# Optimization experiments

Measured on AMD Instinct MI355X. Metric: run time of the kernel, lower is better.

The kernel has to match this reference:

```python
import jax, jax.numpy as jnp
import numpy as np

N = 100_000   # nodes
E = 1_600_000 # edges
V = 100_000   # vocab
G = 256       # graphs in batch
D = 64        # emb/hidden dim


def setup_inputs() -> dict:
    key = jax.random.key(0)
    ks = jax.random.split(key, 12)
    x_tokens = jax.random.randint(ks[0], (N, 1), 0, V)
    edge_index = jax.random.randint(ks[1], (2, E), 0, N)
    batch = jnp.sort(jax.random.randint(ks[2], (N,), 0, G))
    s = 0.02
    return {
        "x_tokens": x_tokens,
        "edge_index": edge_index,
        "batch": batch,
        "emb_table": jax.random.normal(ks[3], (V, D), jnp.float32) * s,
        "W0": jax.random.normal(ks[4], (D, D), jnp.float32) * s,
        "b0": jnp.zeros((D,), jnp.float32),
        "W1": jax.random.normal(ks[5], (D, D), jnp.float32) * s,
        "b1": jnp.zeros((D,), jnp.float32),
        "W2": jax.random.normal(ks[6], (D, D), jnp.float32) * s,
        "b2": jnp.zeros((D,), jnp.float32),
        "Wc1": jax.random.normal(ks[7], (2 * D, D), jnp.float32) * s,
        "bc1": jnp.zeros((D,), jnp.float32),
        "Wc2": jax.random.normal(ks[8], (D, 2), jnp.float32) * s,
        "bc2": jnp.zeros((2,), jnp.float32),
    }


def _gcn_norm(edge_index, n_nodes):
    # add self loops, compute symmetric normalization coefficients
    loop = jnp.arange(n_nodes, dtype=edge_index.dtype)
    src = jnp.concatenate([edge_index[0], loop])
    dst = jnp.concatenate([edge_index[1], loop])
    deg = jax.ops.segment_sum(jnp.ones_like(dst, jnp.float32), dst, num_segments=n_nodes)
    dinv = jnp.where(deg > 0, deg ** -0.5, 0.0)
    norm = dinv[src] * dinv[dst]  # [E+N]
    return src, dst, norm


def _gcn_conv(x, W, b, src, dst, norm, n_nodes):
    x = x @ W                                   # [N, D]
    msg = x[src] * norm[:, None]                # gather + scale, [E+N, D]
    out = jax.ops.segment_sum(msg, dst, num_segments=n_nodes)
    return out + b


def reference(x_tokens, edge_index, batch, emb_table, W0, b0, W1, b1, W2, b2, Wc1, bc1, Wc2, bc2):
    n = x_tokens.shape[0]
    src, dst, norm = _gcn_norm(edge_index, n)
    x = emb_table[x_tokens[:, 0]]               # [N, D]
    for W, b in ((W0, b0), (W1, b1), (W2, b2)):
        x = jax.nn.relu(_gcn_conv(x, W, b, src, dst, norm, n))
    # dual pooling over graph ids
    cnt = jax.ops.segment_sum(jnp.ones((n,), x.dtype), batch, num_segments=G)
    h_sum = jax.ops.segment_sum(x, batch, num_segments=G)
    h_mean = h_sum / jnp.maximum(cnt, 1.0)[:, None]
    h_max = jax.ops.segment_max(x, batch, num_segments=G)
    h_max = jnp.where(jnp.isfinite(h_max), h_max, 0.0)
    h = jnp.concatenate([h_mean, h_max], axis=-1)   # [G, 2D]
    logits = jax.nn.relu(h @ Wc1 + bc1) @ Wc2 + bc2  # [G, 2]
    return logits
```

## Files before the change

### kernel.cpp

```cpp
#include <hip/hip_runtime.h>
#include <hip/hip_fp16.h>
#include <math.h>


#define BKT_LOG 9
#define BKT (1 << BKT_LOG)
#define CHUNK 4096

typedef _Float16 h2 __attribute__((ext_vector_type(2)));
typedef _Float16 f16x4 __attribute__((ext_vector_type(4)));
typedef _Float16 f16x8 __attribute__((ext_vector_type(8)));
typedef float f32x4 __attribute__((ext_vector_type(4)));

union HU { unsigned u; h2 h; };
__device__ inline h2 h2bits(unsigned u) { HU x; x.u = u; return x.h; }

#if __has_builtin(__builtin_amdgcn_fdot2)
#define FDOT2(a, b, c) __builtin_amdgcn_fdot2((a), (b), (c), false)
#else
__device__ inline float FDOT2(h2 a, h2 b, float c) {
  return (float)a.x * (float)b.x + (float)a.y * (float)b.y + c;
}
#endif

#define MASK_X 0x00003C00u
#define MASK_Y 0x3C000000u

__device__ inline void acc4c(uint2 v, float& a0, float& a1, float& a2, float& a3) {
  h2 lo = h2bits(v.x), hi = h2bits(v.y);
  a0 = FDOT2(lo, h2bits(MASK_X), a0);
  a1 = FDOT2(lo, h2bits(MASK_Y), a1);
  a2 = FDOT2(hi, h2bits(MASK_X), a2);
  a3 = FDOT2(hi, h2bits(MASK_Y), a3);
}

__global__ __launch_bounds__(256) void k_wcvt(const float* __restrict__ W0,
                                              const float* __restrict__ W1,
                                              const float* __restrict__ W2,
                                              _Float16* __restrict__ Wf,
                                              int* __restrict__ gcur,
                                              float* __restrict__ hz, int hzn) {
  if (blockIdx.x < 3) {
    const float* W = (blockIdx.x == 0) ? W0 : (blockIdx.x == 1) ? W1 : W2;
    _Float16* out = Wf + blockIdx.x * 4096;
    for (int i = threadIdx.x; i < 4096; i += 256) {
      int c = i >> 10, s = (i >> 9) & 1, l = (i >> 3) & 63, j = i & 7;
      int k = 32 * s + 8 * (l >> 4) + j;
      int ncol = 16 * c + (l & 15);
      out[i] = (_Float16)W[k * 64 + ncol];
    }
  } else if (blockIdx.x == 3) {
    gcur[threadIdx.x] = 0;
  } else {
    for (int i = threadIdx.x; i < hzn; i += 256) hz[i] = 0.f;
  }
}

__global__ __launch_bounds__(256) void k_part(const int* __restrict__ src,
                                              const int* __restrict__ dst,
                                              int* __restrict__ gcur,
                                              int* __restrict__ ebuf,
                                              int E, int S) {
  __shared__ int sA[CHUNK];
  __shared__ int dA[CHUNK];
  __shared__ int h[256], base[256];
  int tid = threadIdx.x;
  long c0 = (long)blockIdx.x * CHUNK;
  int m = (int)min((long)CHUNK, (long)E - c0);
  h[tid] = 0;
  __syncthreads();
  for (int i = tid; i < m; i += 256) {
    int s = src[c0 + i];
    int d = dst[c0 + i];
    sA[i] = s;
    dA[i] = d;
    atomicAdd(&h[d >> BKT_LOG], 1);
  }
  __syncthreads();
  if (h[tid]) base[tid] = atomicAdd(&gcur[tid], h[tid]);
  __syncthreads();
  h[tid] = 0;
  __syncthreads();
  for (int i = tid; i < m; i += 256) {
    int s = sA[i], d = dA[i];
    int k = d >> BKT_LOG;
    int p = base[k] + atomicAdd(&h[k], 1);
    if (p < S)
      ebuf[k * S + p] = ((d & (BKT - 1)) << 17) | s;
  }
}

__global__ __launch_bounds__(512) void k_bplace(const int* __restrict__ ebuf,
                                                const int* __restrict__ gcur,
                                                int* __restrict__ off,
                                                int* __restrict__ eend,
                                                int* __restrict__ csrc,
                                                float* __restrict__ dinv,
                                                int N, int S) {
  __shared__ int s[512];
  __shared__ int cur[512];
  int b = blockIdx.x, tid = threadIdx.x;
  int n0 = b << BKT_LOG;
  int nn = min(BKT, N - n0);
  int e0 = b * S;
  int cnt = min(gcur[b], S - nn);
  s[tid] = (tid < nn) ? 1 : 0;
  __syncthreads();
  for (int e = tid; e < cnt; e += 512) atomicAdd(&s[ebuf[e0 + e] >> 17], 1);
  __syncthreads();
  int degws = s[tid];
  for (int d = 1; d < 512; d <<= 1) {
    int t = (tid >= d) ? s[tid - d] : 0;
    __syncthreads();
    s[tid] += t;
    __syncthreads();
  }
  int excl = s[tid] - degws;
  if (tid < nn) {
    off[n0 + tid] = e0 + excl;
    eend[n0 + tid] = e0 + excl + degws;
    dinv[n0 + tid] = 1.0f / sqrtf((float)degws);
    csrc[e0 + excl] = n0 + tid;
  }
  cur[tid] = excl + ((tid < nn) ? 1 : 0);
  __syncthreads();
  for (int e = tid; e < cnt; e += 512) {
    int p = ebuf[e0 + e];
    int pos = e0 + atomicAdd(&cur[p >> 17], 1);
    csrc[pos] = p & 0x1FFFF;
  }
}

template <bool EMB>
__global__ __launch_bounds__(256) void k_mfmamm(const _Float16* __restrict__ y,
                                                const int* __restrict__ tok,
                                                const float* __restrict__ emb,
                                                const _Float16* __restrict__ Wf,
                                                const float* __restrict__ dinv,
                                                float scale,
                                                _Float16* __restrict__ xh,
                                                int n) {
  __shared__ _Float16 lds[4 * 16 * 72];
  int w = threadIdx.x >> 6, l = threadIdx.x & 63;
  int m = l & 15, q = l >> 4;
  int rbase = blockIdx.x * 64 + w * 16;

  f16x8 a0, a1;
  if (EMB) {
    int node = min(rbase + m, n - 1);
    const float* er = emb + (size_t)tok[node] * 64;
    float4 v0 = *(const float4*)(er + q * 8);
    float4 v1 = *(const float4*)(er + q * 8 + 4);
    float4 v2 = *(const float4*)(er + 32 + q * 8);
    float4 v3 = *(const float4*)(er + 32 + q * 8 + 4);
    a0[0] = (_Float16)v0.x; a0[1] = (_Float16)v0.y; a0[2] = (_Float16)v0.z; a0[3] = (_Float16)v0.w;
    a0[4] = (_Float16)v1.x; a0[5] = (_Float16)v1.y; a0[6] = (_Float16)v1.z; a0[7] = (_Float16)v1.w;
    a1[0] = (_Float16)v2.x; a1[1] = (_Float16)v2.y; a1[2] = (_Float16)v2.z; a1[3] = (_Float16)v2.w;
    a1[4] = (_Float16)v3.x; a1[5] = (_Float16)v3.y; a1[6] = (_Float16)v3.z; a1[7] = (_Float16)v3.w;
  } else {
    int node = rbase + m;
    const _Float16* yr = y + ((size_t)(unsigned)node << 6);
    a0 = *(const f16x8*)(yr + q * 8);
    a1 = *(const f16x8*)(yr + 32 + q * 8);
  }
  float4 d4 = *(const float4*)(dinv + rbase + q * 4);

  const f16x8* wf = (const f16x8*)Wf + l;
  f32x4 acc[4];
#pragma unroll
  for (int c = 0; c < 4; c++) {
    f32x4 z = {0.f, 0.f, 0.f, 0.f};
    z = __builtin_amdgcn_mfma_f32_16x16x32_f16(a0, wf[(c * 2 + 0) * 64], z, 0, 0, 0);
    z = __builtin_amdgcn_mfma_f32_16x16x32_f16(a1, wf[(c * 2 + 1) * 64], z, 0, 0, 0);
    acc[c] = z;
  }

  const float ds[4] = {d4.x * scale, d4.y * scale, d4.z * scale, d4.w * scale};
  _Float16* ldw = lds + w * 16 * 72;
#pragma unroll
  for (int c = 0; c < 4; c++)
#pragma unroll
    for (int r = 0; r < 4; r++)
      ldw[(q * 4 + r) * 72 + c * 16 + m] = (_Float16)(acc[c][r] * ds[r]);
  __syncthreads();

  int row2 = l & 15, c2 = l >> 4;
  int node = rbase + row2;
  if (node < n) {
    const uint4* s4 = (const uint4*)(ldw + row2 * 72 + c2 * 16);
    uint4 v0 = s4[0], v1 = s4[1];
    uint4* dst = (uint4*)(xh + ((size_t)(unsigned)node << 6) + c2 * 16);
    dst[0] = v0;
    dst[1] = v1;
  }
}

__global__ __launch_bounds__(256) void k_aggregate(const int* __restrict__ off,
                                                   const int* __restrict__ eend,
                                                   const int* __restrict__ csrc,
                                                   const float* __restrict__ dinv,
                                                   const _Float16* __restrict__ xh,
                                                   const float* __restrict__ bias,
                                                   _Float16* __restrict__ outp,
                                                   int n) {
  int lane = threadIdx.x & 63;
  int t = blockIdx.x * 4 + (threadIdx.x >> 6);
  if (t >= n) return;
  int e0 = off[t];
  int e1 = eend[t];
  int p = lane >> 4;
  int f = lane & 15;
  const char* xb = (const char*)xh;

  float a0 = 0.f, a1 = 0.f, a2 = 0.f, a3 = 0.f;
  for (int base = (e0 & ~7); base < e1; base += 32) {
    int my = base + p * 8;
    int4 iA = {0, 0, 0, 0}, iB = {0, 0, 0, 0};
    if (my < e1) iA = *(const int4*)(csrc + my);
    if (my + 4 < e1) iB = *(const int4*)(csrc + my + 4);
    uint2 v0 = {0,0}, v1 = {0,0}, v2 = {0,0}, v3 = {0,0};
    uint2 v4 = {0,0}, v5 = {0,0}, v6 = {0,0}, v7 = {0,0};
    if (my + 0 >= e0 && my + 0 < e1) v0 = *(const uint2*)(xb + ((size_t)(unsigned)iA.x << 7) + f * 8);
    if (my + 1 >= e0 && my + 1 < e1) v1 = *(const uint2*)(xb + ((size_t)(unsigned)iA.y << 7) + f * 8);
    if (my + 2 >= e0 && my + 2 < e1) v2 = *(const uint2*)(xb + ((size_t)(unsigned)iA.z << 7) + f * 8);
    if (my + 3 >= e0 && my + 3 < e1) v3 = *(const uint2*)(xb + ((size_t)(unsigned)iA.w << 7) + f * 8);
    if (my + 4 >= e0 && my + 4 < e1) v4 = *(const uint2*)(xb + ((size_t)(unsigned)iB.x << 7) + f * 8);
    if (my + 5 >= e0 && my + 5 < e1) v5 = *(const uint2*)(xb + ((size_t)(unsigned)iB.y << 7) + f * 8);
    if (my + 6 >= e0 && my + 6 < e1) v6 = *(const uint2*)(xb + ((size_t)(unsigned)iB.z << 7) + f * 8);
    if (my + 7 >= e0 && my + 7 < e1) v7 = *(const uint2*)(xb + ((size_t)(unsigned)iB.w << 7) + f * 8);
    acc4c(v0, a0, a1, a2, a3);
    acc4c(v1, a0, a1, a2, a3);
    acc4c(v2, a0, a1, a2, a3);
    acc4c(v3, a0, a1, a2, a3);
    acc4c(v4, a0, a1, a2, a3);
    acc4c(v5, a0, a1, a2, a3);
    acc4c(v6, a0, a1, a2, a3);
    acc4c(v7, a0, a1, a2, a3);
  }

  a0 += __shfl_xor(a0, 16); a0 += __shfl_xor(a0, 32);
  a1 += __shfl_xor(a1, 16); a1 += __shfl_xor(a1, 32);
  a2 += __shfl_xor(a2, 16); a2 += __shfl_xor(a2, 32);
  a3 += __shfl_xor(a3, 16); a3 += __shfl_xor(a3, 32);

  if (p == 0) {
    float sc = dinv[t] * (1.0f / 256.0f);
    float4 bb = *(const float4*)(bias + f * 4);
    f16x4 hv;
    hv[0] = (_Float16)(fmaxf(a0 * sc + bb.x, 0.f) * 4096.f);
    hv[1] = (_Float16)(fmaxf(a1 * sc + bb.y, 0.f) * 4096.f);
    hv[2] = (_Float16)(fmaxf(a2 * sc + bb.z, 0.f) * 4096.f);
    hv[3] = (_Float16)(fmaxf(a3 * sc + bb.w, 0.f) * 4096.f);
    *(f16x4*)((char*)outp + ((size_t)(unsigned)t << 7) + f * 8) = hv;
  }
}

__global__ __launch_bounds__(256) void k_pool(const _Float16* __restrict__ x,
                                              const int* __restrict__ batch,
                                              float* __restrict__ hsum,
                                              float* __restrict__ hmax,
                                              int* __restrict__ cntg,
                                              int n) {
  int wid = (blockIdx.x * blockDim.x + threadIdx.x) >> 6;
  int lane = threadIdx.x & 63;
  int i0 = wid * 64;
  if (i0 >= n) return;
  int i1 = min(i0 + 64, n);
  int batch_l = (i0 + lane < n) ? batch[i0 + lane] : 0;
  float gsum = 0.f, gmax = 0.f;
  int cur = __shfl(batch_l, 0);
  int c = 0;
  for (int i = i0; i < i1; i++) {
    int g = __shfl(batch_l, i - i0);
    if (g != cur) {
      atomicAdd(&hsum[cur * 64 + lane], gsum);
      atomicMax((int*)&hmax[cur * 64 + lane], __float_as_int(gmax));
      if (lane == 0) atomicAdd(&cntg[cur], c);
      gsum = 0.f; gmax = 0.f; c = 0; cur = g;
    }
    float v = (float)x[((size_t)(unsigned)i << 6) + lane];
    gsum += v;
    gmax = fmaxf(gmax, v);
    c++;
  }
  atomicAdd(&hsum[cur * 64 + lane], gsum);
  atomicMax((int*)&hmax[cur * 64 + lane], __float_as_int(gmax));
  if (lane == 0) atomicAdd(&cntg[cur], c);
}

__global__ __launch_bounds__(64) void k_cls(const float* __restrict__ hsum,
                                            const float* __restrict__ hmax,
                                            const int* __restrict__ cnt,
                                            const float* __restrict__ Wc1,
                                            const float* __restrict__ bc1,
                                            const float* __restrict__ Wc2,
                                            const float* __restrict__ bc2,
                                            float* __restrict__ out) {
  __shared__ float h[128];
  __shared__ float hid[64];
  int g = blockIdx.x, j = threadIdx.x;
  int c = cnt[g];
  float cf = (float)(c > 0 ? c : 1);
  h[j] = hsum[g * 64 + j] / cf * (1.0f / 4096.0f);
  h[64 + j] = hmax[g * 64 + j] * (1.0f / 4096.0f);
  __syncthreads();
  float acc = bc1[j];
  for (int k = 0; k < 128; k++) acc += h[k] * Wc1[k * 64 + j];
  hid[j] = fmaxf(acc, 0.f);
  __syncthreads();
  if (j < 2) {
    float a = bc2[j];
    for (int k = 0; k < 64; k++) a += hid[k] * Wc2[k * 2 + j];
    out[g * 2 + j] = a;
  }
}

extern "C" void kernel_launch(void* const* d_in, const int* in_sizes, int n_in,
                              void* d_out, int out_size, void* d_ws, size_t ws_size,
                              hipStream_t stream) {
  const int N = in_sizes[0];
  const int E = in_sizes[1] / 2;
  const int G = out_size / 2;
  const int B = (N + BKT - 1) >> BKT_LOG;
  const int Npad = (N + 63) & ~63;
  const int S = ((((E + B - 1) / B) * 3 / 2 + 256) + 7) & ~7;

  const int* tok   = (const int*)d_in[0];
  const int* ei    = (const int*)d_in[1];
  const int* batch = (const int*)d_in[2];
  const float* emb = (const float*)d_in[3];
  const float* W0 = (const float*)d_in[4];  const float* b0 = (const float*)d_in[5];
  const float* W1 = (const float*)d_in[6];  const float* b1 = (const float*)d_in[7];
  const float* W2 = (const float*)d_in[8];  const float* b2 = (const float*)d_in[9];
  const float* Wc1 = (const float*)d_in[10]; const float* bc1 = (const float*)d_in[11];
  const float* Wc2 = (const float*)d_in[12]; const float* bc2 = (const float*)d_in[13];
  const int* srcp = ei;
  const int* dstp = ei + E;

  int* off    = (int*)d_ws;
  int* eend   = off + N;
  float* dinv = (float*)(eend + N);
  int* gcur   = (int*)(dinv + Npad);
  _Float16* Wf = (_Float16*)(gcur + 256);
  int* csrc   = (int*)(Wf + 3 * 4096);
  _Float16* xh = (_Float16*)(csrc + (size_t)B * S);
  _Float16* y  = xh + (size_t)Npad * 64;
  int* ebuf   = (int*)y;
  float* hsum = (float*)(y + (size_t)Npad * 64);
  float* hmax = hsum + (size_t)G * 64;
  int*   cntg = (int*)(hmax + (size_t)G * 64);

  auto cdiv = [](long a, long b) { return (int)((a + b - 1) / b); };
  const int aggBlocks = cdiv(N, 4);

  k_wcvt<<<5, 256, 0, stream>>>(W0, W1, W2, Wf, gcur, hsum, G * 129);

  k_part<<<cdiv(E, CHUNK), 256, 0, stream>>>(srcp, dstp, gcur, ebuf, E, S);
  k_bplace<<<B, 512, 0, stream>>>(ebuf, gcur, off, eend, csrc, dinv, N, S);

  k_mfmamm<true><<<cdiv(N, 64), 256, 0, stream>>>(nullptr, tok, emb, Wf, dinv, 256.f, xh, N);
  k_aggregate<<<aggBlocks, 256, 0, stream>>>(off, eend, csrc, dinv, xh, b0, y, N);

  k_mfmamm<false><<<cdiv(N, 64), 256, 0, stream>>>(y, nullptr, nullptr, Wf + 4096, dinv, 1.f / 16.f, xh, N);
  k_aggregate<<<aggBlocks, 256, 0, stream>>>(off, eend, csrc, dinv, xh, b1, y, N);

  k_mfmamm<false><<<cdiv(N, 64), 256, 0, stream>>>(y, nullptr, nullptr, Wf + 8192, dinv, 1.f / 16.f, xh, N);
  k_aggregate<<<aggBlocks, 256, 0, stream>>>(off, eend, csrc, dinv, xh, b2, y, N);

  k_pool<<<cdiv(N, 256), 256, 0, stream>>>(y, batch, hsum, hmax, cntg, N);

  k_cls<<<G, 64, 0, stream>>>(hsum, hmax, cntg, Wc1, bc1, Wc2, bc2, (float*)d_out);
}
```

Baseline: 332.3 us.

## Locally sort edges by bucket in k_part and split aggregate launches in halves

After: 345.1 us. +3.8%, slower.

```diff
diff --git a/kernel.cpp b/kernel.cpp
--- a/kernel.cpp
+++ b/kernel.cpp
@@ -61,9 +61,10 @@
                                               int* __restrict__ gcur,
                                               int* __restrict__ ebuf,
                                               int E, int S) {
-  __shared__ int sA[CHUNK];
-  __shared__ int dA[CHUNK];
-  __shared__ int h[256], base[256];
+  __shared__ int pk[CHUNK];
+  __shared__ unsigned short bk[CHUNK];
+  __shared__ unsigned short sp[CHUNK];
+  __shared__ int h[256], sc[256], base[256], cur[256];
   int tid = threadIdx.x;
   long c0 = (long)blockIdx.x * CHUNK;
   int m = (int)min((long)CHUNK, (long)E - c0);
@@ -72,21 +73,37 @@
   for (int i = tid; i < m; i += 256) {
     int s = src[c0 + i];
     int d = dst[c0 + i];
-    sA[i] = s;
-    dA[i] = d;
-    atomicAdd(&h[d >> BKT_LOG], 1);
-  }
-  __syncthreads();
-  if (h[tid]) base[tid] = atomicAdd(&gcur[tid], h[tid]);
-  __syncthreads();
-  h[tid] = 0;
+    int b = d >> BKT_LOG;
+    pk[i] = ((d & (BKT - 1)) << 17) | s;
+    bk[i] = (unsigned short)b;
+    atomicAdd(&h[b], 1);
+  }
+  __syncthreads();
+  int hv = h[tid];
+  if (hv) base[tid] = atomicAdd(&gcur[tid], hv);
+  sc[tid] = hv;
+  __syncthreads();
+  for (int d = 1; d < 256; d <<= 1) {
+    int t = (tid >= d) ? sc[tid - d] : 0;
+    __syncthreads();
+    sc[tid] += t;
+    __syncthreads();
+  }
+  cur[tid] = sc[tid] - hv;
   __syncthreads();
   for (int i = tid; i < m; i += 256) {
-    int s = sA[i], d = dA[i];
-    int k = d >> BKT_LOG;
-    int p = base[k] + atomicAdd(&h[k], 1);
-    if (p < S)
-      ebuf[k * S + p] = ((d & (BKT - 1)) << 17) | s;
+    int p = atomicAdd(&cur[bk[i]], 1);
+    sp[p] = (unsigned short)i;
+  }
+  __syncthreads();
+  for (int j = tid; j < m; j += 256) {
+    int lo = 0, hi = 255;
+    while (lo < hi) { int mid = (lo + hi) >> 1; if (sc[mid] > j) hi = mid; else lo = mid + 1; }
+    int b = lo;
+    int rel = j - (sc[b] - h[b]);
+    int gpos = base[b] + rel;
+    if (gpos < S)
+      ebuf[(size_t)b * S + gpos] = pk[sp[j]];
   }
 }
 
@@ -202,10 +219,10 @@
                                                    const _Float16* __restrict__ xh,
                                                    const float* __restrict__ bias,
                                                    _Float16* __restrict__ outp,
-                                                   int n) {
+                                                   int n0w, int n1) {
   int lane = threadIdx.x & 63;
-  int t = blockIdx.x * 4 + (threadIdx.x >> 6);
-  if (t >= n) return;
+  int t = __builtin_amdgcn_readfirstlane(n0w + blockIdx.x * 4 + (threadIdx.x >> 6));
+  if (t >= n1) return;
   int e0 = off[t];
   int e1 = eend[t];
   int p = lane >> 4;
@@ -351,7 +368,8 @@
   int*   cntg = (int*)(hmax + (size_t)G * 64);
 
   auto cdiv = [](long a, long b) { return (int)((a + b - 1) / b); };
-  const int aggBlocks = cdiv(N, 4);
+  const int Nh = (N / 2 + 3) & ~3;
+  const int agA = cdiv(Nh, 4), agB = cdiv(N - Nh, 4);
 
   k_wcvt<<<5, 256, 0, stream>>>(W0, W1, W2, Wf, gcur, hsum, G * 129);
 
@@ -359,13 +377,16 @@
   k_bplace<<<B, 512, 0, stream>>>(ebuf, gcur, off, eend, csrc, dinv, N, S);
 
   k_mfmamm<true><<<cdiv(N, 64), 256, 0, stream>>>(nullptr, tok, emb, Wf, dinv, 256.f, xh, N);
-  k_aggregate<<<aggBlocks, 256, 0, stream>>>(off, eend, csrc, dinv, xh, b0, y, N);
+  k_aggregate<<<agA, 256, 0, stream>>>(off, eend, csrc, dinv, xh, b0, y, 0, Nh);
+  k_aggregate<<<agB, 256, 0, stream>>>(off, eend, csrc, dinv, xh, b0, y, Nh, N);
 
   k_mfmamm<false><<<cdiv(N, 64), 256, 0, stream>>>(y, nullptr, nullptr, Wf + 4096, dinv, 1.f / 16.f, xh, N);
-  k_aggregate<<<aggBlocks, 256, 0, stream>>>(off, eend, csrc, dinv, xh, b1, y, N);
+  k_aggregate<<<agA, 256, 0, stream>>>(off, eend, csrc, dinv, xh, b1, y, 0, Nh);
+  k_aggregate<<<agB, 256, 0, stream>>>(off, eend, csrc, dinv, xh, b1, y, Nh, N);
 
   k_mfmamm<false><<<cdiv(N, 64), 256, 0, stream>>>(y, nullptr, nullptr, Wf + 8192, dinv, 1.f / 16.f, xh, N);
-  k_aggregate<<<aggBlocks, 256, 0, stream>>>(off, eend, csrc, dinv, xh, b2, y, N);
+  k_aggregate<<<agA, 256, 0, stream>>>(off, eend, csrc, dinv, xh, b2, y, 0, Nh);
+  k_aggregate<<<agB, 256, 0, stream>>>(off, eend, csrc, dinv, xh, b2, y, Nh, N);
 
   k_pool<<<cdiv(N, 256), 256, 0, stream>>>(y, batch, hsum, hmax, cntg, N);
 
```
